# Kernel optimization log

Measured on AMD Instinct MI355X. Metric: run time of the kernel, lower is better.

The kernel has to match this reference:

```python
import jax, jax.numpy as jnp
import numpy as np

DEPTH = 4  # signature truncation depth
B, L, D = 64, 2048, 8  # batch, path length, channels


def _exp_levels(z, depth):
    """Restricted tensor exponential of a single linear increment.

    z: (B, d). Returns tuple of flattened z^{(x)k} / k!, shapes (B, d**k).
    """
    b = z.shape[0]
    levels = [z]
    for k in range(2, depth + 1):
        prev = levels[-1]  # (B, d**(k-1))
        levels.append((prev[:, :, None] * z[:, None, :]).reshape(b, -1) / k)
    return tuple(levels)


def _signature(path, depth):
    """Truncated path signature of a piecewise-linear path.

    Signature = product (in the truncated tensor algebra) of exp(increment_i),
    combined left-to-right via Chen's identity.
    path: (B, L, d) -> (B, d + d^2 + ... + d^depth)
    """
    inc = path[:, 1:, :] - path[:, :-1, :]  # (B, L-1, d)
    b = path.shape[0]

    def chen_mul_exp(A, z):
        # (A tensor-product exp(z)) truncated at `depth`.
        # C_k = A_k + e_k + sum_{j=1}^{k-1} A_{k-j} (x) e_j,  e_j = z^{(x)j}/j!
        e = _exp_levels(z, depth)
        out = []
        for k in range(1, depth + 1):
            c = A[k - 1] + e[k - 1]
            for j in range(1, k):
                c = c + (A[k - j - 1][:, :, None] * e[j - 1][:, None, :]).reshape(b, -1)
            out.append(c)
        return tuple(out)

    init = _exp_levels(inc[:, 0], depth)          # signature of first segment
    rest = jnp.swapaxes(inc[:, 1:], 0, 1)          # (L-2, B, d), scan over time
    final, _ = jax.lax.scan(lambda c, z: (chen_mul_exp(c, z), None), init, rest)
    return jnp.concatenate(final, axis=-1)         # flatten: (B, d + ... + d^depth)


def setup_inputs() -> dict:
    key = jax.random.key(0)
    path = jax.random.normal(key, (B, L, D), dtype=jnp.float32)
    return {"path": path}


def reference(path):
    return _signature(path, DEPTH)
```

## Files before the change

kernel.cpp:

```cpp
#include <hip/hip_runtime.h>

#define D8      8
#define LPATH   2048
#define NBATCH  64
#define NSTEPS  2047
#define CSTEPS  64
#define NCHUNK  32
#define SIGLEN  4680
#define OFF2    8
#define OFF3    72
#define OFF4    584
#define P4      68
#define SIGP    (OFF4 + 64 * P4)
#define ZPITCH  68
#define APITCH  40
#define BROWS   80

typedef float  f32x4 __attribute__((ext_vector_type(4)));
typedef short  s16x8 __attribute__((ext_vector_type(8)));

__device__ __forceinline__ void load8(const float* __restrict__ p, float* v) {
    float4 a = ((const float4*)p)[0];
    float4 b = ((const float4*)p)[1];
    v[0]=a.x; v[1]=a.y; v[2]=a.z; v[3]=a.w;
    v[4]=b.x; v[5]=b.y; v[6]=b.z; v[7]=b.w;
}
__device__ __forceinline__ void store8(float* __restrict__ p, const float* v) {
    ((float4*)p)[0] = make_float4(v[0],v[1],v[2],v[3]);
    ((float4*)p)[1] = make_float4(v[4],v[5],v[6],v[7]);
}
__device__ __forceinline__ unsigned int f2bf(float f) {
    unsigned int u = __builtin_bit_cast(unsigned int, f);
    u += 0x7FFFu + ((u >> 16) & 1u);
    return u >> 16;
}

__device__ __forceinline__ void one_step(float Zi, float Zj,
                                         float& A2, float& a1i, float& Wl,
                                         float& c3o, float& c4o, float& h3o, float& h4o) {
    const float p  = Zi * Zj;
    const float uq = a1i * Zj;
    c4o = fmaf(uq, 1.f/6.f, fmaf(p, 1.f/24.f, A2 * 0.5f));
    c3o = fmaf(uq, 0.5f,    fmaf(p, 1.f/6.f,  A2));
    Wl -= Zj;
    h3o = Zi * Wl;
    h4o = p;
    A2 = A2 + fmaf(p, 0.5f, uq);
    a1i += Zi;
}

__global__ __launch_bounds__(512) void sig_group_kernel(const float* __restrict__ path,
                                                        float* __restrict__ gsigs) {
    __shared__ __align__(16) float          zt[8][8 * ZPITCH];
    __shared__ __align__(16) unsigned short Al[8][64 * APITCH];
    __shared__ __align__(16) unsigned short Bl[8][BROWS * APITCH];
    __shared__ __align__(16) float          SB[SIGP];

    const int w    = threadIdx.x >> 6;
    const int lane = threadIdx.x & 63;
    const int G    = blockIdx.x & 3;
    const int b    = blockIdx.x >> 2;
    const int c    = G * 8 + w;
    const int t0   = c * CSTEPS;
    const int t1   = (t0 + CSTEPS < NSTEPS) ? (t0 + CSTEPS) : NSTEPS;
    const int n    = t1 - t0;
    const int i    = lane >> 3;
    const int j    = lane & 7;
    const float* __restrict__ pb = path + (size_t)b * LPATH * D8;

    float* __restrict__ zw = &zt[w][0];
    unsigned short* __restrict__ Aw = &Al[w][0];
    unsigned short* __restrict__ Bw = &Bl[w][0];

    {
        float z8[8];
        if (lane < n) {
            const float* s0 = pb + (size_t)(t0 + lane) * D8;
            float a0[8], a1v[8];
            load8(s0, a0); load8(s0 + D8, a1v);
#pragma unroll
            for (int m = 0; m < 8; ++m) z8[m] = a1v[m] - a0[m];
        } else {
#pragma unroll
            for (int m = 0; m < 8; ++m) z8[m] = 0.f;
        }
#pragma unroll
        for (int m = 0; m < 8; ++m) zw[m * ZPITCH + lane] = z8[m];

        const uint4 zz = make_uint4(0u, 0u, 0u, 0u);
        *(uint4*)(Bw + 64 * APITCH + lane * 8) = zz;
        if (lane < 16) *(uint4*)(Bw + 64 * APITCH + 512 + lane * 8) = zz;
    }

    const float Tj = pb[(size_t)t1 * D8 + j] - pb[(size_t)t0 * D8 + j];

    float A2 = 0.f, a1i = 0.f, Wl = Tj;
    f32x4 acc[4][5];
#pragma unroll
    for (int rt = 0; rt < 4; ++rt)
#pragma unroll
        for (int ct = 0; ct < 5; ++ct)
            acc[rt][ct] = (f32x4){0.f, 0.f, 0.f, 0.f};

    for (int pass = 0; pass < 4; ++pass) {
        const int p16 = pass * 16;
#pragma unroll
        for (int bt = 0; bt < 2; ++bt) {
            const int sb8 = p16 + bt * 8;
            f32x4 zia = *(const f32x4*)(zw + i * ZPITCH + sb8);
            f32x4 zib = *(const f32x4*)(zw + i * ZPITCH + sb8 + 4);
            f32x4 zja = *(const f32x4*)(zw + j * ZPITCH + sb8);
            f32x4 zjb = *(const f32x4*)(zw + j * ZPITCH + sb8 + 4);

            unsigned int c3pk[4], c4pk[4], h3pk[4], h4pk[4];
#pragma unroll
            for (int t = 0; t < 4; ++t) {
                const float Zi0 = (2*t   < 4) ? zia[(2*t)   & 3] : zib[(2*t)   & 3];
                const float Zi1 = (2*t+1 < 4) ? zia[(2*t+1) & 3] : zib[(2*t+1) & 3];
                const float Zj0 = (2*t   < 4) ? zja[(2*t)   & 3] : zjb[(2*t)   & 3];
                const float Zj1 = (2*t+1 < 4) ? zja[(2*t+1) & 3] : zjb[(2*t+1) & 3];
                float c3a, c4a, h3a, h4a, c3b, c4b, h3b, h4b;
                one_step(Zi0, Zj0, A2, a1i, Wl, c3a, c4a, h3a, h4a);
                one_step(Zi1, Zj1, A2, a1i, Wl, c3b, c4b, h3b, h4b);
                c3pk[t] = f2bf(c3a) | (f2bf(c3b) << 16);
                c4pk[t] = f2bf(c4a) | (f2bf(c4b) << 16);
                h3pk[t] = f2bf(h3a) | (f2bf(h3b) << 16);
                h4pk[t] = f2bf(h4a) | (f2bf(h4b) << 16);
            }
            *(uint4*)(Aw + lane * APITCH + bt * 8)      = make_uint4(c3pk[0], c3pk[1], c3pk[2], c3pk[3]);
            *(uint4*)(Aw + lane * APITCH + 16 + bt * 8) = make_uint4(c4pk[0], c4pk[1], c4pk[2], c4pk[3]);
            *(uint4*)(Bw + lane * APITCH + bt * 8)      = make_uint4(h3pk[0], h3pk[1], h3pk[2], h3pk[3]);
            *(uint4*)(Bw + lane * APITCH + 16 + bt * 8) = make_uint4(h4pk[0], h4pk[1], h4pk[2], h4pk[3]);
            if (j == 0) {
                const unsigned int z0 = f2bf(zia[0]) | (f2bf(zia[1]) << 16);
                const unsigned int z1 = f2bf(zia[2]) | (f2bf(zia[3]) << 16);
                const unsigned int z2 = f2bf(zib[0]) | (f2bf(zib[1]) << 16);
                const unsigned int z3 = f2bf(zib[2]) | (f2bf(zib[3]) << 16);
                *(uint4*)(Bw + (64 + i) * APITCH + bt * 8) = make_uint4(z0, z1, z2, z3);
            }
        }
        s16x8 af[4], bfr[5];
#pragma unroll
        for (int rt = 0; rt < 4; ++rt)
            af[rt] = *(const s16x8*)(Aw + (rt * 16 + (lane & 15)) * APITCH + (lane >> 4) * 8);
#pragma unroll
        for (int ct = 0; ct < 5; ++ct)
            bfr[ct] = *(const s16x8*)(Bw + (ct * 16 + (lane & 15)) * APITCH + (lane >> 4) * 8);
#pragma unroll
        for (int rt = 0; rt < 4; ++rt)
#pragma unroll
            for (int ct = 0; ct < 5; ++ct)
                acc[rt][ct] = __builtin_amdgcn_mfma_f32_16x16x32_bf16(af[rt], bfr[ct], acc[rt][ct], 0, 0, 0);
    }

    const int r0 = (lane >> 4) * 4;
    const int cl = lane & 15;

    float FA4[8], fa3, FA1[8], FA2, fa1i;

    __syncthreads();
    for (int s = 0; s < 8; ++s) {
        if (w == s) {
            if ((lane & 7) == 0) SB[lane >> 3] = a1i;
            SB[OFF2 + lane] = A2;
            if (cl < 8) {
#pragma unroll
                for (int rt = 0; rt < 4; ++rt)
#pragma unroll
                    for (int reg = 0; reg < 4; ++reg)
                        SB[OFF3 + (rt * 16 + r0 + reg) * 8 + cl] = acc[rt][4][reg];
            }
#pragma unroll
            for (int rt = 0; rt < 4; ++rt)
#pragma unroll
                for (int ct = 0; ct < 4; ++ct)
#pragma unroll
                    for (int reg = 0; reg < 4; ++reg)
                        SB[OFF4 + (rt * 16 + r0 + reg) * P4 + ct * 16 + cl] = acc[rt][ct][reg];
        }
        __syncthreads();
        if (s == 0) {
            load8(SB, FA1);
            fa1i = SB[i];
            FA2  = SB[OFF2 + lane];
            fa3  = SB[OFF3 + lane * 8 + w];
            load8(SB + OFF4 + lane * P4 + w * 8, FA4);
        } else {
            float B1[8]; load8(SB, B1);
            const float b1i = SB[i];
            const float b1j = SB[j];
            const float b2t = SB[OFF2 + lane];
            const float b1k = SB[w];
            const float b3k = SB[OFF3 + lane * 8 + w];
            const float b2jk = SB[OFF2 + j * 8 + w];
            float b4r[8], b2r[8], b3r[8];
            load8(SB + OFF4 + lane * P4 + w * 8, b4r);
            load8(SB + OFF2 + w * 8,             b2r);
            load8(SB + OFF3 + (j * 8 + w) * 8,   b3r);
#pragma unroll
            for (int l = 0; l < 8; ++l) {
                float v = FA4[l] + b4r[l];
                v = fmaf(fa3,  B1[l], v);
                v = fmaf(FA2,  b2r[l], v);
                FA4[l] = fmaf(fa1i, b3r[l], v);
            }
            fa3 = fmaf(fa1i, b2jk, fmaf(FA2, b1k, fa3 + b3k));
            FA2 = FA2 + fmaf(fa1i, b1j, b2t);
#pragma unroll
            for (int m = 0; m < 8; ++m) FA1[m] += B1[m];
            fa1i += b1i;
        }
        __syncthreads();
    }

    float* __restrict__ o = gsigs + (size_t)blockIdx.x * SIGLEN;
    if (w == 0) {
        if (lane < 8) o[lane] = FA1[lane];
        o[OFF2 + lane] = FA2;
    }
    o[OFF3 + lane * 8 + w] = fa3;
    store8(o + OFF4 + lane * 64 + w * 8, FA4);
}

struct BSet {
    float B1[8], b4r[8], b2r[8], b3r[8];
    float b1i, b1j, b2t, b1k, b3k, b2jk;
};

__device__ __forceinline__ void loadB(BSet& S, const float* __restrict__ B,
                                      int lane, int i, int j, int k) {
    load8(B, S.B1);
    S.b1i = B[i];
    S.b1j = B[j];
    S.b2t = B[OFF2 + lane];
    S.b1k = B[k];
    S.b3k = B[OFF3 + lane * 8 + k];
    S.b2jk = B[OFF2 + j * 8 + k];
    load8(B + OFF4 + lane * 64 + k * 8, S.b4r);
    load8(B + OFF2 + k * 8,             S.b2r);
    load8(B + OFF3 + j * 64 + k * 8,    S.b3r);
}

__device__ __forceinline__ void applyB(const BSet& S, float (&A4)[8], float& a3s,
                                       float (&A1)[8], float& A2, float& a1i) {
#pragma unroll
    for (int l = 0; l < 8; ++l) {
        float v = A4[l] + S.b4r[l];
        v = fmaf(a3s, S.B1[l], v);
        v = fmaf(A2,  S.b2r[l], v);
        A4[l] = fmaf(a1i, S.b3r[l], v);
    }
    a3s = fmaf(a1i, S.b2jk, fmaf(A2, S.b1k, a3s + S.b3k));
    A2 = A2 + fmaf(a1i, S.b1j, S.b2t);
#pragma unroll
    for (int m = 0; m < 8; ++m) A1[m] += S.B1[m];
    a1i += S.b1i;
}

template<int NPER>
__global__ __launch_bounds__(512) void sig_combine_kernel(const float* __restrict__ in,
                                                          float* __restrict__ out) {
    const int grp  = blockIdx.x;
    const int tid  = threadIdx.x;
    const int w    = tid >> 6;
    const int lane = tid & 63;
    const int i    = lane >> 3;
    const int j    = lane & 7;
    const int k    = w;
    const float* __restrict__ base = in + (size_t)grp * NPER * SIGLEN;

    float A4[8], a3s, A1[8], A2, a1i;
    load8(base, A1);
    a1i = base[i];
    A2  = base[OFF2 + lane];
    a3s = base[OFF3 + lane * 8 + k];
    load8(base + OFF4 + lane * 64 + k * 8, A4);

    BSet Sa, Sb;
    int s = 1;
    loadB(Sa, base + (size_t)s * SIGLEN, lane, i, j, k);
    while (s + 1 < NPER) {
        loadB(Sb, base + (size_t)(s + 1) * SIGLEN, lane, i, j, k);
        applyB(Sa, A4, a3s, A1, A2, a1i);
        ++s;
        if (s + 1 < NPER)
            loadB(Sa, base + (size_t)(s + 1) * SIGLEN, lane, i, j, k);
        applyB(Sb, A4, a3s, A1, A2, a1i);
        ++s;
    }
    if (s < NPER)
        applyB(Sa, A4, a3s, A1, A2, a1i);

    float* __restrict__ o = out + (size_t)grp * SIGLEN;
    if (w == 0) {
        if (lane < 8) o[lane] = A1[lane];
        o[OFF2 + lane] = A2;
    }
    o[OFF3 + lane * 8 + k] = a3s;
    store8(o + OFF4 + lane * 64 + k * 8, A4);
}

extern "C" void kernel_launch(void* const* d_in, const int* in_sizes, int n_in,
                              void* d_out, int out_size, void* d_ws, size_t ws_size,
                              hipStream_t stream) {
    const float* path = (const float*)d_in[0];
    float* out   = (float*)d_out;
    float* gsigs = (float*)d_ws;

    sig_group_kernel<<<NBATCH * 4, 512, 0, stream>>>(path, gsigs);
    sig_combine_kernel<4><<<NBATCH, 512, 0, stream>>>(gsigs, out);
}
```

Measured before the change: 31.31 us.

## Split each chunk across two waves and use smaller two-chunk blocks

Each 64-step chunk is now computed by two wavefronts. One builds the A operands and the other builds the B operands, and each wave runs half of the MFMA row tiles. Blocks shrink to 256 threads covering two chunks, so there are 16 groups per batch instead of 4 and shared memory is reused through a single aliased buffer. The intent is more parallelism and occupancy and a shorter serial in-block combine (2 stages instead of 8). The cost is extra __syncthreads per pass and a combine kernel that must merge 16 partial signatures per batch instead of 4.

Result: slower. 50.20 us (+60.3%).

```diff
diff --git a/kernel.cpp b/kernel.cpp
--- a/kernel.cpp
+++ b/kernel.cpp
@@ -5,16 +5,22 @@
 #define NBATCH  64
 #define NSTEPS  2047
 #define CSTEPS  64
-#define NCHUNK  32
 #define SIGLEN  4680
 #define OFF2    8
 #define OFF3    72
+#define A3P     72
+#define SOFF4   (OFF3 + 8 * A3P)
+#define P4      68
+#define SIGP    (SOFF4 + 64 * P4)
 #define OFF4    584
-#define P4      68
-#define SIGP    (OFF4 + 64 * P4)
 #define ZPITCH  68
 #define APITCH  40
 #define BROWS   80
+
+#define A_OFF   0
+#define B_OFF   10240
+#define Z_OFF   23040
+#define SMEM_BYTES 27392
 
 typedef float  f32x4 __attribute__((ext_vector_type(4)));
 typedef short  s16x8 __attribute__((ext_vector_type(8)));
@@ -49,18 +55,18 @@
     a1i += Zi;
 }
 
-__global__ __launch_bounds__(512) void sig_group_kernel(const float* __restrict__ path,
-                                                        float* __restrict__ gsigs) {
-    __shared__ __align__(16) float          zt[8][8 * ZPITCH];
-    __shared__ __align__(16) unsigned short Al[8][64 * APITCH];
-    __shared__ __align__(16) unsigned short Bl[8][BROWS * APITCH];
-    __shared__ __align__(16) float          SB[SIGP];
-
-    const int w    = threadIdx.x >> 6;
-    const int lane = threadIdx.x & 63;
-    const int G    = blockIdx.x & 3;
-    const int b    = blockIdx.x >> 2;
-    const int c    = G * 8 + w;
+__global__ __launch_bounds__(256) void sig_pair_kernel(const float* __restrict__ path,
+                                                       float* __restrict__ gsigs) {
+    __shared__ __align__(16) unsigned char smem[SMEM_BYTES];
+
+    const int tid  = threadIdx.x;
+    const int w    = tid >> 6;
+    const int cw   = w >> 1;
+    const int h    = w & 1;
+    const int lane = tid & 63;
+    const int g    = blockIdx.x & 15;
+    const int b    = blockIdx.x >> 4;
+    const int c    = g * 2 + cw;
     const int t0   = c * CSTEPS;
     const int t1   = (t0 + CSTEPS < NSTEPS) ? (t0 + CSTEPS) : NSTEPS;
     const int n    = t1 - t0;
@@ -68,11 +74,12 @@
     const int j    = lane & 7;
     const float* __restrict__ pb = path + (size_t)b * LPATH * D8;
 
-    float* __restrict__ zw = &zt[w][0];
-    unsigned short* __restrict__ Aw = &Al[w][0];
-    unsigned short* __restrict__ Bw = &Bl[w][0];
-
-    {
+    unsigned short* __restrict__ Aw = (unsigned short*)(smem + A_OFF) + cw * (64 * APITCH);
+    unsigned short* __restrict__ Bw = (unsigned short*)(smem + B_OFF) + cw * (BROWS * APITCH);
+    float* __restrict__ zw = (float*)(smem + Z_OFF) + cw * (8 * ZPITCH);
+    float* __restrict__ SB = (float*)smem;
+
+    if (h == 0) {
         float z8[8];
         if (lane < n) {
             const float* s0 = pb + (size_t)(t0 + lane) * D8;
@@ -86,18 +93,19 @@
         }
 #pragma unroll
         for (int m = 0; m < 8; ++m) zw[m * ZPITCH + lane] = z8[m];
-
+    } else {
         const uint4 zz = make_uint4(0u, 0u, 0u, 0u);
         *(uint4*)(Bw + 64 * APITCH + lane * 8) = zz;
         if (lane < 16) *(uint4*)(Bw + 64 * APITCH + 512 + lane * 8) = zz;
     }
+    __syncthreads();
 
     const float Tj = pb[(size_t)t1 * D8 + j] - pb[(size_t)t0 * D8 + j];
 
     float A2 = 0.f, a1i = 0.f, Wl = Tj;
-    f32x4 acc[4][5];
-#pragma unroll
-    for (int rt = 0; rt < 4; ++rt)
+    f32x4 acc[2][5];
+#pragma unroll
+    for (int rt = 0; rt < 2; ++rt)
 #pragma unroll
         for (int ct = 0; ct < 5; ++ct)
             acc[rt][ct] = (f32x4){0.f, 0.f, 0.f, 0.f};
@@ -127,84 +135,98 @@
                 h3pk[t] = f2bf(h3a) | (f2bf(h3b) << 16);
                 h4pk[t] = f2bf(h4a) | (f2bf(h4b) << 16);
             }
-            *(uint4*)(Aw + lane * APITCH + bt * 8)      = make_uint4(c3pk[0], c3pk[1], c3pk[2], c3pk[3]);
-            *(uint4*)(Aw + lane * APITCH + 16 + bt * 8) = make_uint4(c4pk[0], c4pk[1], c4pk[2], c4pk[3]);
-            *(uint4*)(Bw + lane * APITCH + bt * 8)      = make_uint4(h3pk[0], h3pk[1], h3pk[2], h3pk[3]);
-            *(uint4*)(Bw + lane * APITCH + 16 + bt * 8) = make_uint4(h4pk[0], h4pk[1], h4pk[2], h4pk[3]);
-            if (j == 0) {
-                const unsigned int z0 = f2bf(zia[0]) | (f2bf(zia[1]) << 16);
-                const unsigned int z1 = f2bf(zia[2]) | (f2bf(zia[3]) << 16);
-                const unsigned int z2 = f2bf(zib[0]) | (f2bf(zib[1]) << 16);
-                const unsigned int z3 = f2bf(zib[2]) | (f2bf(zib[3]) << 16);
-                *(uint4*)(Bw + (64 + i) * APITCH + bt * 8) = make_uint4(z0, z1, z2, z3);
+            if (h == 0) {
+                *(uint4*)(Aw + lane * APITCH + bt * 8)      = make_uint4(c3pk[0], c3pk[1], c3pk[2], c3pk[3]);
+                *(uint4*)(Aw + lane * APITCH + 16 + bt * 8) = make_uint4(c4pk[0], c4pk[1], c4pk[2], c4pk[3]);
+            } else {
+                *(uint4*)(Bw + lane * APITCH + bt * 8)      = make_uint4(h3pk[0], h3pk[1], h3pk[2], h3pk[3]);
+                *(uint4*)(Bw + lane * APITCH + 16 + bt * 8) = make_uint4(h4pk[0], h4pk[1], h4pk[2], h4pk[3]);
+                if (j == 0) {
+                    const unsigned int z0 = f2bf(zia[0]) | (f2bf(zia[1]) << 16);
+                    const unsigned int z1 = f2bf(zia[2]) | (f2bf(zia[3]) << 16);
+                    const unsigned int z2 = f2bf(zib[0]) | (f2bf(zib[1]) << 16);
+                    const unsigned int z3 = f2bf(zib[2]) | (f2bf(zib[3]) << 16);
+                    *(uint4*)(Bw + (64 + i) * APITCH + bt * 8) = make_uint4(z0, z1, z2, z3);
+                }
             }
         }
-        s16x8 af[4], bfr[5];
-#pragma unroll
-        for (int rt = 0; rt < 4; ++rt)
-            af[rt] = *(const s16x8*)(Aw + (rt * 16 + (lane & 15)) * APITCH + (lane >> 4) * 8);
+        __syncthreads();
+        s16x8 af[2], bfr[5];
+#pragma unroll
+        for (int rt = 0; rt < 2; ++rt)
+            af[rt] = *(const s16x8*)(Aw + (((2*h + rt) * 16) + (lane & 15)) * APITCH + (lane >> 4) * 8);
 #pragma unroll
         for (int ct = 0; ct < 5; ++ct)
             bfr[ct] = *(const s16x8*)(Bw + (ct * 16 + (lane & 15)) * APITCH + (lane >> 4) * 8);
 #pragma unroll
-        for (int rt = 0; rt < 4; ++rt)
+        for (int rt = 0; rt < 2; ++rt)
 #pragma unroll
             for (int ct = 0; ct < 5; ++ct)
                 acc[rt][ct] = __builtin_amdgcn_mfma_f32_16x16x32_bf16(af[rt], bfr[ct], acc[rt][ct], 0, 0, 0);
+        __syncthreads();
     }
 
     const int r0 = (lane >> 4) * 4;
     const int cl = lane & 15;
-
-    float FA4[8], fa3, FA1[8], FA2, fa1i;
-
-    __syncthreads();
-    for (int s = 0; s < 8; ++s) {
-        if (w == s) {
-            if ((lane & 7) == 0) SB[lane >> 3] = a1i;
-            SB[OFF2 + lane] = A2;
+    const int k0 = 2 * w;
+    float FA4[2][8], fa3[2], FA1[8], FA2, fa1i;
+
+    for (int s = 0; s < 2; ++s) {
+        if (cw == s) {
+            if (h == 0) {
+                if ((lane & 7) == 0) SB[lane >> 3] = a1i;
+                SB[OFF2 + lane] = A2;
+            }
             if (cl < 8) {
 #pragma unroll
-                for (int rt = 0; rt < 4; ++rt)
+                for (int rt = 0; rt < 2; ++rt)
+#pragma unroll
+                    for (int reg = 0; reg < 4; ++reg) {
+                        const int row = (2*h + rt) * 16 + r0 + reg;
+                        SB[OFF3 + (row >> 3) * A3P + (row & 7) * 8 + cl] = acc[rt][4][reg];
+                    }
+            }
+#pragma unroll
+            for (int rt = 0; rt < 2; ++rt)
+#pragma unroll
+                for (int ct = 0; ct < 4; ++ct)
 #pragma unroll
                     for (int reg = 0; reg < 4; ++reg)
-                        SB[OFF3 + (rt * 16 + r0 + reg) * 8 + cl] = acc[rt][4][reg];
-            }
-#pragma unroll
-            for (int rt = 0; rt < 4; ++rt)
-#pragma unroll
-                for (int ct = 0; ct < 4; ++ct)
-#pragma unroll
-                    for (int reg = 0; reg < 4; ++reg)
-                        SB[OFF4 + (rt * 16 + r0 + reg) * P4 + ct * 16 + cl] = acc[rt][ct][reg];
+                        SB[SOFF4 + ((2*h + rt) * 16 + r0 + reg) * P4 + ct * 16 + cl] = acc[rt][ct][reg];
         }
         __syncthreads();
         if (s == 0) {
             load8(SB, FA1);
             fa1i = SB[i];
             FA2  = SB[OFF2 + lane];
-            fa3  = SB[OFF3 + lane * 8 + w];
-            load8(SB + OFF4 + lane * P4 + w * 8, FA4);
+            fa3[0] = SB[OFF3 + i * A3P + j * 8 + k0];
+            fa3[1] = SB[OFF3 + i * A3P + j * 8 + k0 + 1];
+            load8(SB + SOFF4 + lane * P4 + k0 * 8,       FA4[0]);
+            load8(SB + SOFF4 + lane * P4 + (k0 + 1) * 8, FA4[1]);
         } else {
             float B1[8]; load8(SB, B1);
             const float b1i = SB[i];
             const float b1j = SB[j];
             const float b2t = SB[OFF2 + lane];
-            const float b1k = SB[w];
-            const float b3k = SB[OFF3 + lane * 8 + w];
-            const float b2jk = SB[OFF2 + j * 8 + w];
-            float b4r[8], b2r[8], b3r[8];
-            load8(SB + OFF4 + lane * P4 + w * 8, b4r);
-            load8(SB + OFF2 + w * 8,             b2r);
-            load8(SB + OFF3 + (j * 8 + w) * 8,   b3r);
-#pragma unroll
-            for (int l = 0; l < 8; ++l) {
-                float v = FA4[l] + b4r[l];
-                v = fmaf(fa3,  B1[l], v);
-                v = fmaf(FA2,  b2r[l], v);
-                FA4[l] = fmaf(fa1i, b3r[l], v);
-            }
-            fa3 = fmaf(fa1i, b2jk, fmaf(FA2, b1k, fa3 + b3k));
+#pragma unroll
+            for (int kk = 0; kk < 2; ++kk) {
+                const int k = k0 + kk;
+                const float b1k  = SB[k];
+                const float b3k  = SB[OFF3 + i * A3P + j * 8 + k];
+                const float b2jk = SB[OFF2 + j * 8 + k];
+                float b4r[8], b2r[8], b3r[8];
+                load8(SB + SOFF4 + lane * P4 + k * 8, b4r);
+                load8(SB + OFF2 + k * 8,              b2r);
+                load8(SB + OFF3 + j * A3P + k * 8,    b3r);
+#pragma unroll
+                for (int l = 0; l < 8; ++l) {
+                    float v = FA4[kk][l] + b4r[l];
+                    v = fmaf(fa3[kk], B1[l], v);
+                    v = fmaf(FA2,     b2r[l], v);
+                    FA4[kk][l] = fmaf(fa1i, b3r[l], v);
+                }
+                fa3[kk] = fmaf(fa1i, b2jk, fmaf(FA2, b1k, fa3[kk] + b3k));
+            }
             FA2 = FA2 + fmaf(fa1i, b1j, b2t);
 #pragma unroll
             for (int m = 0; m < 8; ++m) FA1[m] += B1[m];
@@ -218,8 +240,9 @@
         if (lane < 8) o[lane] = FA1[lane];
         o[OFF2 + lane] = FA2;
     }
-    o[OFF3 + lane * 8 + w] = fa3;
-    store8(o + OFF4 + lane * 64 + w * 8, FA4);
+    *(float2*)(o + OFF3 + lane * 8 + k0) = make_float2(fa3[0], fa3[1]);
+    store8(o + OFF4 + lane * 64 + k0 * 8,       FA4[0]);
+    store8(o + OFF4 + lane * 64 + (k0 + 1) * 8, FA4[1]);
 }
 
 struct BSet {
@@ -307,6 +330,6 @@
     float* out   = (float*)d_out;
     float* gsigs = (float*)d_ws;
 
-    sig_group_kernel<<<NBATCH * 4, 512, 0, stream>>>(path, gsigs);
-    sig_combine_kernel<4><<<NBATCH, 512, 0, stream>>>(gsigs, out);
-}
+    sig_pair_kernel<<<NBATCH * 16, 256, 0, stream>>>(path, gsigs);
+    sig_combine_kernel<16><<<NBATCH, 512, 0, stream>>>(gsigs, out);
+}
```
